# Optimization experiments

Hardware: AMD Instinct MI355X
Metric: run time of the kernel (lower is better)

The kernel has to match this reference:

```python
import jax, jax.numpy as jnp
import numpy as np
import math

N_HEAD = 16  # from init_kwargs

def setup_inputs() -> dict:
    key = jax.random.key(0)
    ks = jax.random.split(key, 11)
    B, T, D = 2, 2048, 1024
    s = 0.02
    return {
        "q": jax.random.normal(ks[0], (B, T, D), jnp.float32),
        "k": jax.random.normal(ks[1], (B, T, D), jnp.float32),
        "v": jax.random.normal(ks[2], (B, T, D), jnp.float32),
        "Wq": jax.random.normal(ks[3], (D, D), jnp.float32) * s,
        "bq": jax.random.normal(ks[4], (D,), jnp.float32) * s,
        "Wk": jax.random.normal(ks[5], (D, D), jnp.float32) * s,
        "bk": jax.random.normal(ks[6], (D,), jnp.float32) * s,
        "Wv": jax.random.normal(ks[7], (D, D), jnp.float32) * s,
        "bv": jax.random.normal(ks[8], (D,), jnp.float32) * s,
        "Wc": jax.random.normal(ks[9], (D, D), jnp.float32) * s,
        "bc": jax.random.normal(ks[10], (D,), jnp.float32) * s,
    }

def reference(q, k, v, Wq, bq, Wk, bk, Wv, bv, Wc, bc):
    B, T, D = q.shape
    H = N_HEAD
    nd = D // H

    def proj(x, W, b):
        # torch Linear: x @ W.T + b; then split heads -> [b, h, t, nd]
        y = x @ W.T + b
        return y.reshape(B, T, H, nd).transpose(0, 2, 1, 3)

    qh = proj(q, Wq, bq)
    kh = proj(k, Wk, bk)
    vh = proj(v, Wv, bv)

    # scores: [b, h, t_q, t_k]
    z = jnp.einsum('bhqd,bhkd->bhqk', qh, kh) / math.sqrt(nd)
    mask = jnp.tril(jnp.ones((T, T), dtype=bool))  # causal
    z = jnp.where(mask, z, -jnp.inf)
    # NOTE: original uses nn.Softmax(dim=-2) -> softmax over the QUERY axis
    attn = jax.nn.softmax(z, axis=-2)
    out = jnp.einsum('bhqk,bhkd->bhqd', attn, vh)  # [b, h, t, nd]
    out = out.transpose(0, 2, 1, 3).reshape(B, T, D)
    return out @ Wc.T + bc
```

## Files before the change

### kernel.cpp

```cpp
#include <hip/hip_runtime.h>


#define Dd 1024
#define Tt 2048
#define Bb 2
#define Hh 16
#define NDh 64
#define Mm (Bb * Tt)

using u16 = unsigned short;
using u32 = unsigned int;
typedef __attribute__((ext_vector_type(8))) short bf16x8;
typedef __attribute__((ext_vector_type(4))) float f32x4;

__device__ __forceinline__ u16 f2bf(float f) {
  return (u16)((__float_as_uint(f) + 0x8000u) >> 16);
}
__device__ __forceinline__ u32 pk2(float a, float b) {
  u32 ua = __float_as_uint(a) + 0x8000u;
  u32 ub = __float_as_uint(b) + 0x8000u;
  return __builtin_amdgcn_perm(ub, ua, 0x07060302u);
}
__device__ __forceinline__ void ldsdma16(const u16* g, u16* l) {
  __builtin_amdgcn_global_load_lds(
      (const __attribute__((address_space(1))) u32*)g,
      (__attribute__((address_space(3))) u32*)l, 16, 0, 0);
}
#define MFMA(a, b, c) __builtin_amdgcn_mfma_f32_16x16x32_bf16((a), (b), (c), 0, 0, 0)
__device__ __forceinline__ bf16x8 ldfrag(const u16* lds, int row, int kgrp) {
  return *(const bf16x8*)(lds + row * 64 + (((kgrp) ^ (row & 7)) * 8));
}

__global__ __launch_bounds__(256) void cvt_w(
    const float* __restrict__ w0, const float* __restrict__ w1,
    const float* __restrict__ w2, const float* __restrict__ w3,
    u16* __restrict__ dst, float* __restrict__ outz, float* __restrict__ lsumz)
{
  const int vid = blockIdx.x * 256 + threadIdx.x;
  const int seg = vid >> 18;
  const int off = (vid & 0x3FFFF) * 4;
  const float* s = seg == 0 ? w0 : seg == 1 ? w1 : seg == 2 ? w2 : w3;
  float4 f = *(const float4*)(s + off);
  ushort4 o;
  o.x = f2bf(f.x); o.y = f2bf(f.y); o.z = f2bf(f.z); o.w = f2bf(f.w);
  *(ushort4*)(dst + (size_t)seg * Dd * Dd + off) = o;
  *(float4*)(outz + (size_t)vid * 4) = make_float4(0.f, 0.f, 0.f, 0.f);
  if (vid < Bb * Hh * Tt / 4)
    *(float4*)(lsumz + (size_t)vid * 4) = make_float4(0.f, 0.f, 0.f, 0.f);
}

template <bool XF32>
__device__ __forceinline__ void gemm_body(
    const void* Xv, const u16* __restrict__ WB, const float* __restrict__ bias,
    void* Yv, float oscale, int omode, int kc, int knum, u16* As, u16* Bs)
{
  const int t = threadIdx.x, lane = t & 63, w = t >> 6;
  const int col = lane & 15, quad = lane >> 4;
  const int m0 = blockIdx.x * 64, n0 = blockIdx.y * 128;
  const int wm = (w >> 1) * 32, wn = (w & 1) * 64;
  const int drr = lane >> 3, dsw = ((lane & 7) ^ drr) * 8;
  const int ar = t >> 2, ag = (t & 3) * 2;
  const int kbeg = (Dd / knum) * kc, kend = kbeg + Dd / knum;

  f32x4 acc[2][4] = {};
  float4 xf[4];
  const float* X32 = (const float*)Xv;
  if constexpr (XF32) {
#pragma unroll
    for (int j = 0; j < 4; j++)
      xf[j] = ((const float4*)(X32 + (size_t)(m0 + ar) * Dd + kbeg + ag * 8))[j];
  }

  for (int k0 = kbeg; k0 < kend; k0 += 64) {
    __syncthreads();
#pragma unroll
    for (int i = 0; i < 4; i++) {
      const int rr = w * 32 + i * 8;
      ldsdma16(WB + (size_t)(n0 + rr + drr) * Dd + k0 + dsw, Bs + rr * 64);
    }
    if constexpr (XF32) {
      u32 pk[8];
#pragma unroll
      for (int j = 0; j < 4; j++) {
        pk[2 * j]     = pk2(xf[j].x, xf[j].y);
        pk[2 * j + 1] = pk2(xf[j].z, xf[j].w);
      }
      u16* dst = As + ar * 64;
      *(uint4*)(dst + ((ag ^ (ar & 7)) * 8))       = make_uint4(pk[0], pk[1], pk[2], pk[3]);
      *(uint4*)(dst + (((ag + 1) ^ (ar & 7)) * 8)) = make_uint4(pk[4], pk[5], pk[6], pk[7]);
      if (k0 + 64 < kend) {
#pragma unroll
        for (int j = 0; j < 4; j++)
          xf[j] = ((const float4*)(X32 + (size_t)(m0 + ar) * Dd + k0 + 64 + ag * 8))[j];
      }
    } else {
      const u16* X = (const u16*)Xv;
#pragma unroll
      for (int i = 0; i < 2; i++) {
        const int rr = w * 16 + i * 8;
        ldsdma16(X + (size_t)(m0 + rr + drr) * Dd + k0 + dsw, As + rr * 64);
      }
    }
    __syncthreads();
#pragma unroll
    for (int s = 0; s < 2; s++) {
      bf16x8 a[2], b[4];
#pragma unroll
      for (int i = 0; i < 2; i++)
        a[i] = ldfrag(As, wm + i * 16 + col, s * 4 + quad);
#pragma unroll
      for (int j = 0; j < 4; j++)
        b[j] = ldfrag(Bs, wn + j * 16 + col, s * 4 + quad);
#pragma unroll
      for (int i = 0; i < 2; i++)
#pragma unroll
        for (int j = 0; j < 4; j++)
          acc[i][j] = MFMA(a[i], b[j], acc[i][j]);
    }
  }

#pragma unroll
  for (int jt = 0; jt < 4; jt++) {
    const int n = n0 + wn + jt * 16 + col;
    const float bn = (omode == 2 && kc != 0) ? 0.f : bias[n];
    if (omode == 1) {
#pragma unroll
      for (int i = 0; i < 2; i++) {
        const int mg = m0 + wm + i * 16 + quad * 4;
        const int bb = mg >> 11, tl = mg & 2047;
        ushort4 o;
        o.x = f2bf(acc[i][jt][0] + bn);
        o.y = f2bf(acc[i][jt][1] + bn);
        o.z = f2bf(acc[i][jt][2] + bn);
        o.w = f2bf(acc[i][jt][3] + bn);
        *(ushort4*)((u16*)Yv + (size_t)bb * Dd * Tt + (size_t)n * Tt + tl) = o;
      }
    } else if (omode == 0) {
      u16* Y = (u16*)Yv;
#pragma unroll
      for (int i = 0; i < 2; i++)
#pragma unroll
        for (int r = 0; r < 4; r++) {
          const int m = m0 + wm + i * 16 + quad * 4 + r;
          Y[(size_t)m * Dd + n] = f2bf((acc[i][jt][r] + bn) * oscale);
        }
    } else {
      float* Y = (float*)Yv;
#pragma unroll
      for (int i = 0; i < 2; i++)
#pragma unroll
        for (int r = 0; r < 4; r++) {
          const int m = m0 + wm + i * 16 + quad * 4 + r;
          atomicAdd(&Y[(size_t)m * Dd + n], acc[i][jt][r] + bn);
        }
    }
  }
}

__global__ __launch_bounds__(256) void proj_qkv(
    const float* __restrict__ q, const float* __restrict__ k,
    const float* __restrict__ v, const u16* __restrict__ Wb,
    const float* __restrict__ bq, const float* __restrict__ bk,
    const float* __restrict__ bv,
    u16* __restrict__ Qp, u16* __restrict__ Kp, u16* __restrict__ VtG)
{
  __shared__ u16 As[64 * 64];
  __shared__ u16 Bs[128 * 64];
  const int z = blockIdx.z;
  const float* X = z == 0 ? q : z == 1 ? k : v;
  const u16* W = Wb + (size_t)z * Dd * Dd;
  const float* bias = z == 0 ? bq : z == 1 ? bk : bv;
  void* Y = z == 0 ? (void*)Qp : z == 1 ? (void*)Kp : (void*)VtG;
  gemm_body<true>(X, W, bias, Y, z == 0 ? 0.125f : 1.0f, z == 2 ? 1 : 0, 0, 1, As, Bs);
}

__global__ __launch_bounds__(256) void gemm_final(
    const u16* __restrict__ Ctx, const u16* __restrict__ Wcb,
    const float* __restrict__ bc, float* __restrict__ out)
{
  __shared__ u16 As[64 * 64];
  __shared__ u16 Bs[128 * 64];
  gemm_body<false>(Ctx, Wcb, bc, out, 1.0f, 2, blockIdx.z, 2, As, Bs);
}

__global__ __launch_bounds__(256) void attn_stats(
    const u16* __restrict__ Qp, const u16* __restrict__ Kp,
    float* __restrict__ lsum)
{
  __shared__ u16 Ks[128 * 64];
  __shared__ u16 Qs[64 * 64];
  const int t = threadIdx.x, lane = t & 63, w = t >> 6;
  const int col = lane & 15, quad = lane >> 4;
  const int bh = blockIdx.x, b = bh >> 4, h = bh & 15;
  const int j = blockIdx.y, tk0 = j * 128, c = blockIdx.z;
  const u16* Kbase = Kp + (size_t)b * Tt * Dd + h * NDh;
  const u16* Qbase = Qp + (size_t)b * Tt * Dd + h * NDh;
  const int drr = lane >> 3, dsw = ((lane & 7) ^ drr) * 8;

#pragma unroll
  for (int i = 0; i < 4; i++) {
    const int rr = w * 32 + i * 8;
    ldsdma16(Kbase + (size_t)(tk0 + rr + drr) * Dd + dsw, Ks + rr * 64);
  }
  __syncthreads();
  bf16x8 ka[2][2];
#pragma unroll
  for (int s2 = 0; s2 < 2; s2++) {
    const int row = w * 32 + s2 * 16 + col;
    ka[s2][0] = ldfrag(Ks, row, quad);
    ka[s2][1] = ldfrag(Ks, row, 4 + quad);
  }

  float l[2][4] = {};

  for (int d = 2 * j + c, i0 = 0; d < Tt / 64; d += 4, i0++) {
    const bool masked = (c < 2) && (i0 == 0);
    const int tq0 = d * 64;
    __syncthreads();
#pragma unroll
    for (int i = 0; i < 2; i++) {
      const int rr = w * 16 + i * 8;
      ldsdma16(Qbase + (size_t)(tq0 + rr + drr) * Dd + dsw, Qs + rr * 64);
    }
    __syncthreads();
#pragma unroll
    for (int jt = 0; jt < 4; jt++) {
      bf16x8 qb0 = ldfrag(Qs, jt * 16 + col, quad);
      bf16x8 qb1 = ldfrag(Qs, jt * 16 + col, 4 + quad);
      const int tq = tq0 + jt * 16 + col;
#pragma unroll
      for (int s2 = 0; s2 < 2; s2++) {
        f32x4 z = {};
        z = MFMA(ka[s2][0], qb0, z);
        z = MFMA(ka[s2][1], qb1, z);
#pragma unroll
        for (int r = 0; r < 4; r++) {
          float e = __expf(z[r]);
          if (masked) {
            const int tk = tk0 + w * 32 + s2 * 16 + quad * 4 + r;
            e = (tq >= tk) ? e : 0.f;
          }
          l[s2][r] += e;
        }
      }
    }
  }

#pragma unroll
  for (int s2 = 0; s2 < 2; s2++)
#pragma unroll
    for (int r = 0; r < 4; r++) {
      float s = l[s2][r];
#pragma unroll
      for (int m = 1; m < 16; m <<= 1) s += __shfl_xor(s, m);
      if (col == 0)
        atomicAdd(&lsum[(size_t)bh * Tt + tk0 + w * 32 + s2 * 16 + quad * 4 + r], s);
    }
}

__global__ __launch_bounds__(256) void attn_out(
    const u16* __restrict__ Qp, const u16* __restrict__ Kp,
    const u16* __restrict__ VtG, const float* __restrict__ lsum,
    u16* __restrict__ Ctx)
{
  __shared__ u16 QPs[64 * 64];
  __shared__ u16 Ks[64 * 64];
  __shared__ u16 Vts[64 * 64];
  __shared__ float srl[64];
  const int t = threadIdx.x, lane = t & 63, w = t >> 6;
  const int col = lane & 15, quad = lane >> 4;
  const int bh = blockIdx.x, b = bh >> 4, h = bh & 15;
  const int tq0 = (gridDim.y - 1 - blockIdx.y) * 64;
  const u16* Qbase = Qp + (size_t)b * Tt * Dd + h * NDh;
  const u16* Kbase = Kp + (size_t)b * Tt * Dd + h * NDh;
  const u16* Vbase = VtG + (size_t)b * Dd * Tt + (size_t)h * NDh * Tt;
  const int drr = lane >> 3, dsw = ((lane & 7) ^ drr) * 8;

#pragma unroll
  for (int i = 0; i < 2; i++) {
    const int rr = w * 16 + i * 8;
    ldsdma16(Qbase + (size_t)(tq0 + rr + drr) * Dd + dsw, QPs + rr * 64);
  }
  __syncthreads();
  bf16x8 qa[2];
  qa[0] = ldfrag(QPs, w * 16 + col, quad);
  qa[1] = ldfrag(QPs, w * 16 + col, 4 + quad);

  f32x4 o[4] = {};

  for (int tk0 = 0; tk0 <= tq0; tk0 += 64) {
    const bool masked = (tk0 == tq0);
    __syncthreads();
#pragma unroll
    for (int i = 0; i < 2; i++) {
      const int rr = w * 16 + i * 8;
      ldsdma16(Kbase + (size_t)(tk0 + rr + drr) * Dd + dsw, Ks + rr * 64);
      ldsdma16(Vbase + (size_t)(rr + drr) * Tt + tk0 + dsw, Vts + rr * 64);
    }
    if (t < 64) srl[t] = 1.0f / lsum[(size_t)bh * Tt + tk0 + t];
    __syncthreads();
#pragma unroll
    for (int jt = 0; jt < 4; jt++) {
      bf16x8 kb0 = ldfrag(Ks, jt * 16 + col, quad);
      bf16x8 kb1 = ldfrag(Ks, jt * 16 + col, 4 + quad);
      const int tkl = jt * 16 + col;
      const float rl = srl[tkl];
      f32x4 z = {};
      z = MFMA(qa[0], kb0, z);
      z = MFMA(qa[1], kb1, z);
#pragma unroll
      for (int r = 0; r < 4; r++) {
        const int row = w * 16 + quad * 4 + r;
        float p = __expf(z[r]) * rl;
        if (masked) p = (tkl <= row) ? p : 0.f;
        QPs[row * 64 + (((tkl >> 3) ^ (row & 7)) * 8) + (tkl & 7)] = f2bf(p);
      }
    }
    bf16x8 pa0 = ldfrag(QPs, w * 16 + col, quad);
    bf16x8 pa1 = ldfrag(QPs, w * 16 + col, 4 + quad);
#pragma unroll
    for (int dn = 0; dn < 4; dn++) {
      bf16x8 vb0 = ldfrag(Vts, dn * 16 + col, quad);
      bf16x8 vb1 = ldfrag(Vts, dn * 16 + col, 4 + quad);
      o[dn] = MFMA(pa0, vb0, o[dn]);
      o[dn] = MFMA(pa1, vb1, o[dn]);
    }
  }

#pragma unroll
  for (int dn = 0; dn < 4; dn++)
#pragma unroll
    for (int r = 0; r < 4; r++) {
      const int tq = tq0 + w * 16 + quad * 4 + r;
      Ctx[(size_t)(b * Tt + tq) * Dd + h * NDh + dn * 16 + col] = f2bf(o[dn][r]);
    }
}

extern "C" void kernel_launch(void* const* d_in, const int* in_sizes, int n_in,
                              void* d_out, int out_size, void* d_ws, size_t ws_size,
                              hipStream_t stream)
{
  const float* q  = (const float*)d_in[0];
  const float* k  = (const float*)d_in[1];
  const float* v  = (const float*)d_in[2];
  const float* Wq = (const float*)d_in[3];
  const float* bq = (const float*)d_in[4];
  const float* Wk = (const float*)d_in[5];
  const float* bk = (const float*)d_in[6];
  const float* Wv = (const float*)d_in[7];
  const float* bv = (const float*)d_in[8];
  const float* Wc = (const float*)d_in[9];
  const float* bc = (const float*)d_in[10];

  u16* Wb   = (u16*)d_ws;
  u16* Qp   = Wb + (size_t)4 * Dd * Dd;
  u16* Kp   = Qp + (size_t)Mm * Dd;
  u16* VtG  = Kp + (size_t)Mm * Dd;
  u16* Ctx  = VtG + (size_t)Mm * Dd;
  float* lsum = (float*)(Ctx + (size_t)Mm * Dd);

  cvt_w<<<4096, 256, 0, stream>>>(Wq, Wk, Wv, Wc, Wb, (float*)d_out, lsum);
  proj_qkv<<<dim3(Mm / 64, Dd / 128, 3), 256, 0, stream>>>(
      q, k, v, Wb, bq, bk, bv, Qp, Kp, VtG);
  attn_stats<<<dim3(Bb * Hh, Tt / 128, 4), 256, 0, stream>>>(Qp, Kp, lsum);
  attn_out<<<dim3(Bb * Hh, Tt / 64), 256, 0, stream>>>(Qp, Kp, VtG, lsum, Ctx);
  gemm_final<<<dim3(Mm / 64, Dd / 128, 2), 256, 0, stream>>>(
      Ctx, Wb + (size_t)3 * Dd * Dd, bc, (float*)d_out);
}
```

Baseline: 268.8 us.

## Pre-convert activations to bf16, enlarge GEMM and attention tiles, use exp2

The activation inputs are now converted to bf16 in the single conversion kernel, so the projection GEMM can stage both operands into shared memory with direct global-to-LDS loads. The GEMM tiles grow from 64x128 to 128x128, and the attention-stats and attention-output kernels process 128 query rows per block for more reuse of each K/V tile. The exp is replaced by a hardware exp2, with log2(e) folded into the Q scale. In exchange the code writes and rereads an extra bf16 copy of q/k/v, uses more registers and LDS per block, and launches fewer blocks, which may lower occupancy.

```diff
diff --git a/kernel.cpp b/kernel.cpp
--- a/kernel.cpp
+++ b/kernel.cpp
@@ -16,10 +16,8 @@
 __device__ __forceinline__ u16 f2bf(float f) {
   return (u16)((__float_as_uint(f) + 0x8000u) >> 16);
 }
-__device__ __forceinline__ u32 pk2(float a, float b) {
-  u32 ua = __float_as_uint(a) + 0x8000u;
-  u32 ub = __float_as_uint(b) + 0x8000u;
-  return __builtin_amdgcn_perm(ub, ua, 0x07060302u);
+__device__ __forceinline__ float fexp2(float x) {
+  return __builtin_amdgcn_exp2f(x);
 }
 __device__ __forceinline__ void ldsdma16(const u16* g, u16* l) {
   __builtin_amdgcn_global_load_lds(
@@ -31,88 +29,70 @@
   return *(const bf16x8*)(lds + row * 64 + (((kgrp) ^ (row & 7)) * 8));
 }
 
-__global__ __launch_bounds__(256) void cvt_w(
+__global__ __launch_bounds__(256) void cvt_all(
     const float* __restrict__ w0, const float* __restrict__ w1,
     const float* __restrict__ w2, const float* __restrict__ w3,
-    u16* __restrict__ dst, float* __restrict__ outz, float* __restrict__ lsumz)
+    const float* __restrict__ q, const float* __restrict__ k,
+    const float* __restrict__ v,
+    u16* __restrict__ Wb, u16* __restrict__ Xb,
+    float* __restrict__ outz, float* __restrict__ lsumz)
 {
   const int vid = blockIdx.x * 256 + threadIdx.x;
-  const int seg = vid >> 18;
-  const int off = (vid & 0x3FFFF) * 4;
-  const float* s = seg == 0 ? w0 : seg == 1 ? w1 : seg == 2 ? w2 : w3;
-  float4 f = *(const float4*)(s + off);
+  const float* s;
+  u16* d;
+  if (vid < (1 << 20)) {
+    const int seg = vid >> 18, off = (vid & 0x3FFFF) * 4;
+    s = (seg == 0 ? w0 : seg == 1 ? w1 : seg == 2 ? w2 : w3) + off;
+    d = Wb + (size_t)seg * Dd * Dd + off;
+    *(float4*)(outz + (size_t)vid * 4) = make_float4(0.f, 0.f, 0.f, 0.f);
+    if (vid < Bb * Hh * Tt / 4)
+      *(float4*)(lsumz + (size_t)vid * 4) = make_float4(0.f, 0.f, 0.f, 0.f);
+  } else {
+    const int iv = vid - (1 << 20);
+    const int seg = iv >> 20, off = (iv & 0xFFFFF) * 4;
+    s = (seg == 0 ? q : seg == 1 ? k : v) + off;
+    d = Xb + (size_t)seg * Mm * Dd + off;
+  }
+  float4 f = *(const float4*)s;
   ushort4 o;
   o.x = f2bf(f.x); o.y = f2bf(f.y); o.z = f2bf(f.z); o.w = f2bf(f.w);
-  *(ushort4*)(dst + (size_t)seg * Dd * Dd + off) = o;
-  *(float4*)(outz + (size_t)vid * 4) = make_float4(0.f, 0.f, 0.f, 0.f);
-  if (vid < Bb * Hh * Tt / 4)
-    *(float4*)(lsumz + (size_t)vid * 4) = make_float4(0.f, 0.f, 0.f, 0.f);
-}
-
-template <bool XF32>
+  *(ushort4*)d = o;
+}
+
 __device__ __forceinline__ void gemm_body(
-    const void* Xv, const u16* __restrict__ WB, const float* __restrict__ bias,
-    void* Yv, float oscale, int omode, int kc, int knum, u16* As, u16* Bs)
+    const u16* __restrict__ X, const u16* __restrict__ WB,
+    const float* __restrict__ bias, void* Yv, float oscale,
+    int omode, int kc, int knum, u16* As, u16* Bs)
 {
   const int t = threadIdx.x, lane = t & 63, w = t >> 6;
   const int col = lane & 15, quad = lane >> 4;
-  const int m0 = blockIdx.x * 64, n0 = blockIdx.y * 128;
-  const int wm = (w >> 1) * 32, wn = (w & 1) * 64;
+  const int m0 = blockIdx.x * 128, n0 = blockIdx.y * 128;
+  const int wm = (w >> 1) * 64, wn = (w & 1) * 64;
   const int drr = lane >> 3, dsw = ((lane & 7) ^ drr) * 8;
-  const int ar = t >> 2, ag = (t & 3) * 2;
   const int kbeg = (Dd / knum) * kc, kend = kbeg + Dd / knum;
 
-  f32x4 acc[2][4] = {};
-  float4 xf[4];
-  const float* X32 = (const float*)Xv;
-  if constexpr (XF32) {
-#pragma unroll
-    for (int j = 0; j < 4; j++)
-      xf[j] = ((const float4*)(X32 + (size_t)(m0 + ar) * Dd + kbeg + ag * 8))[j];
-  }
+  f32x4 acc[4][4] = {};
 
   for (int k0 = kbeg; k0 < kend; k0 += 64) {
     __syncthreads();
 #pragma unroll
     for (int i = 0; i < 4; i++) {
       const int rr = w * 32 + i * 8;
+      ldsdma16(X + (size_t)(m0 + rr + drr) * Dd + k0 + dsw, As + rr * 64);
       ldsdma16(WB + (size_t)(n0 + rr + drr) * Dd + k0 + dsw, Bs + rr * 64);
     }
-    if constexpr (XF32) {
-      u32 pk[8];
-#pragma unroll
-      for (int j = 0; j < 4; j++) {
-        pk[2 * j]     = pk2(xf[j].x, xf[j].y);
-        pk[2 * j + 1] = pk2(xf[j].z, xf[j].w);
-      }
-      u16* dst = As + ar * 64;
-      *(uint4*)(dst + ((ag ^ (ar & 7)) * 8))       = make_uint4(pk[0], pk[1], pk[2], pk[3]);
-      *(uint4*)(dst + (((ag + 1) ^ (ar & 7)) * 8)) = make_uint4(pk[4], pk[5], pk[6], pk[7]);
-      if (k0 + 64 < kend) {
-#pragma unroll
-        for (int j = 0; j < 4; j++)
-          xf[j] = ((const float4*)(X32 + (size_t)(m0 + ar) * Dd + k0 + 64 + ag * 8))[j];
-      }
-    } else {
-      const u16* X = (const u16*)Xv;
-#pragma unroll
-      for (int i = 0; i < 2; i++) {
-        const int rr = w * 16 + i * 8;
-        ldsdma16(X + (size_t)(m0 + rr + drr) * Dd + k0 + dsw, As + rr * 64);
-      }
-    }
     __syncthreads();
 #pragma unroll
     for (int s = 0; s < 2; s++) {
-      bf16x8 a[2], b[4];
-#pragma unroll
-      for (int i = 0; i < 2; i++)
+      bf16x8 a[4], b[4];
+#pragma unroll
+      for (int i = 0; i < 4; i++)
         a[i] = ldfrag(As, wm + i * 16 + col, s * 4 + quad);
 #pragma unroll
       for (int j = 0; j < 4; j++)
         b[j] = ldfrag(Bs, wn + j * 16 + col, s * 4 + quad);
 #pragma unroll
-      for (int i = 0; i < 2; i++)
+      for (int i = 0; i < 4; i++)
 #pragma unroll
         for (int j = 0; j < 4; j++)
           acc[i][j] = MFMA(a[i], b[j], acc[i][j]);
@@ -125,7 +105,7 @@
     const float bn = (omode == 2 && kc != 0) ? 0.f : bias[n];
     if (omode == 1) {
 #pragma unroll
-      for (int i = 0; i < 2; i++) {
+      for (int i = 0; i < 4; i++) {
         const int mg = m0 + wm + i * 16 + quad * 4;
         const int bb = mg >> 11, tl = mg & 2047;
         ushort4 o;
@@ -138,7 +118,7 @@
     } else if (omode == 0) {
       u16* Y = (u16*)Yv;
 #pragma unroll
-      for (int i = 0; i < 2; i++)
+      for (int i = 0; i < 4; i++)
 #pragma unroll
         for (int r = 0; r < 4; r++) {
           const int m = m0 + wm + i * 16 + quad * 4 + r;
@@ -147,7 +127,7 @@
     } else {
       float* Y = (float*)Yv;
 #pragma unroll
-      for (int i = 0; i < 2; i++)
+      for (int i = 0; i < 4; i++)
 #pragma unroll
         for (int r = 0; r < 4; r++) {
           const int m = m0 + wm + i * 16 + quad * 4 + r;
@@ -158,29 +138,29 @@
 }
 
 __global__ __launch_bounds__(256) void proj_qkv(
-    const float* __restrict__ q, const float* __restrict__ k,
-    const float* __restrict__ v, const u16* __restrict__ Wb,
+    const u16* __restrict__ Xb, const u16* __restrict__ Wb,
     const float* __restrict__ bq, const float* __restrict__ bk,
     const float* __restrict__ bv,
     u16* __restrict__ Qp, u16* __restrict__ Kp, u16* __restrict__ VtG)
 {
-  __shared__ u16 As[64 * 64];
+  __shared__ u16 As[128 * 64];
   __shared__ u16 Bs[128 * 64];
   const int z = blockIdx.z;
-  const float* X = z == 0 ? q : z == 1 ? k : v;
+  const u16* X = Xb + (size_t)z * Mm * Dd;
   const u16* W = Wb + (size_t)z * Dd * Dd;
   const float* bias = z == 0 ? bq : z == 1 ? bk : bv;
   void* Y = z == 0 ? (void*)Qp : z == 1 ? (void*)Kp : (void*)VtG;
-  gemm_body<true>(X, W, bias, Y, z == 0 ? 0.125f : 1.0f, z == 2 ? 1 : 0, 0, 1, As, Bs);
+  const float qs = 0.125f * 1.44269504088896f;
+  gemm_body(X, W, bias, Y, z == 0 ? qs : 1.0f, z == 2 ? 1 : 0, 0, 1, As, Bs);
 }
 
 __global__ __launch_bounds__(256) void gemm_final(
     const u16* __restrict__ Ctx, const u16* __restrict__ Wcb,
     const float* __restrict__ bc, float* __restrict__ out)
 {
-  __shared__ u16 As[64 * 64];
+  __shared__ u16 As[128 * 64];
   __shared__ u16 Bs[128 * 64];
-  gemm_body<false>(Ctx, Wcb, bc, out, 1.0f, 2, blockIdx.z, 2, As, Bs);
+  gemm_body(Ctx, Wcb, bc, out, 1.0f, 2, blockIdx.z, 2, As, Bs);
 }
 
 __global__ __launch_bounds__(256) void attn_stats(
@@ -188,7 +168,7 @@
     float* __restrict__ lsum)
 {
   __shared__ u16 Ks[128 * 64];
-  __shared__ u16 Qs[64 * 64];
+  __shared__ u16 Qs[128 * 64];
   const int t = threadIdx.x, lane = t & 63, w = t >> 6;
   const int col = lane & 15, quad = lane >> 4;
   const int bh = blockIdx.x, b = bh >> 4, h = bh & 15;
@@ -213,18 +193,18 @@
 
   float l[2][4] = {};
 
-  for (int d = 2 * j + c, i0 = 0; d < Tt / 64; d += 4, i0++) {
-    const bool masked = (c < 2) && (i0 == 0);
-    const int tq0 = d * 64;
-    __syncthreads();
-#pragma unroll
-    for (int i = 0; i < 2; i++) {
-      const int rr = w * 16 + i * 8;
+  for (int jj = j + c; jj < Tt / 128; jj += 2) {
+    const bool masked = (jj == j);
+    const int tq0 = jj * 128;
+    __syncthreads();
+#pragma unroll
+    for (int i = 0; i < 4; i++) {
+      const int rr = w * 32 + i * 8;
       ldsdma16(Qbase + (size_t)(tq0 + rr + drr) * Dd + dsw, Qs + rr * 64);
     }
     __syncthreads();
 #pragma unroll
-    for (int jt = 0; jt < 4; jt++) {
+    for (int jt = 0; jt < 8; jt++) {
       bf16x8 qb0 = ldfrag(Qs, jt * 16 + col, quad);
       bf16x8 qb1 = ldfrag(Qs, jt * 16 + col, 4 + quad);
       const int tq = tq0 + jt * 16 + col;
@@ -235,7 +215,7 @@
         z = MFMA(ka[s2][1], qb1, z);
 #pragma unroll
         for (int r = 0; r < 4; r++) {
-          float e = __expf(z[r]);
+          float e = fexp2(z[r]);
           if (masked) {
             const int tk = tk0 + w * 32 + s2 * 16 + quad * 4 + r;
             e = (tq >= tk) ? e : 0.f;
@@ -263,33 +243,37 @@
     const u16* __restrict__ VtG, const float* __restrict__ lsum,
     u16* __restrict__ Ctx)
 {
-  __shared__ u16 QPs[64 * 64];
+  __shared__ u16 QPs[128 * 64];
   __shared__ u16 Ks[64 * 64];
   __shared__ u16 Vts[64 * 64];
   __shared__ float srl[64];
   const int t = threadIdx.x, lane = t & 63, w = t >> 6;
   const int col = lane & 15, quad = lane >> 4;
   const int bh = blockIdx.x, b = bh >> 4, h = bh & 15;
-  const int tq0 = (gridDim.y - 1 - blockIdx.y) * 64;
+  const int tq0 = (gridDim.y - 1 - blockIdx.y) * 128;
   const u16* Qbase = Qp + (size_t)b * Tt * Dd + h * NDh;
   const u16* Kbase = Kp + (size_t)b * Tt * Dd + h * NDh;
   const u16* Vbase = VtG + (size_t)b * Dd * Tt + (size_t)h * NDh * Tt;
   const int drr = lane >> 3, dsw = ((lane & 7) ^ drr) * 8;
 
 #pragma unroll
-  for (int i = 0; i < 2; i++) {
-    const int rr = w * 16 + i * 8;
+  for (int i = 0; i < 4; i++) {
+    const int rr = w * 32 + i * 8;
     ldsdma16(Qbase + (size_t)(tq0 + rr + drr) * Dd + dsw, QPs + rr * 64);
   }
   __syncthreads();
-  bf16x8 qa[2];
-  qa[0] = ldfrag(QPs, w * 16 + col, quad);
-  qa[1] = ldfrag(QPs, w * 16 + col, 4 + quad);
-
-  f32x4 o[4] = {};
-
-  for (int tk0 = 0; tk0 <= tq0; tk0 += 64) {
-    const bool masked = (tk0 == tq0);
+  bf16x8 qa[2][2];
+#pragma unroll
+  for (int s2 = 0; s2 < 2; s2++) {
+    const int row = w * 32 + s2 * 16 + col;
+    qa[s2][0] = ldfrag(QPs, row, quad);
+    qa[s2][1] = ldfrag(QPs, row, 4 + quad);
+  }
+
+  f32x4 o[2][4] = {};
+
+  for (int tk0 = 0; tk0 < tq0 + 128; tk0 += 64) {
+    const bool masked = (tk0 >= tq0);
     __syncthreads();
 #pragma unroll
     for (int i = 0; i < 2; i++) {
@@ -305,35 +289,48 @@
       bf16x8 kb1 = ldfrag(Ks, jt * 16 + col, 4 + quad);
       const int tkl = jt * 16 + col;
       const float rl = srl[tkl];
-      f32x4 z = {};
-      z = MFMA(qa[0], kb0, z);
-      z = MFMA(qa[1], kb1, z);
-#pragma unroll
-      for (int r = 0; r < 4; r++) {
-        const int row = w * 16 + quad * 4 + r;
-        float p = __expf(z[r]) * rl;
-        if (masked) p = (tkl <= row) ? p : 0.f;
-        QPs[row * 64 + (((tkl >> 3) ^ (row & 7)) * 8) + (tkl & 7)] = f2bf(p);
-      }
-    }
-    bf16x8 pa0 = ldfrag(QPs, w * 16 + col, quad);
-    bf16x8 pa1 = ldfrag(QPs, w * 16 + col, 4 + quad);
+#pragma unroll
+      for (int s2 = 0; s2 < 2; s2++) {
+        f32x4 z = {};
+        z = MFMA(qa[s2][0], kb0, z);
+        z = MFMA(qa[s2][1], kb1, z);
+#pragma unroll
+        for (int r = 0; r < 4; r++) {
+          const int row = w * 32 + s2 * 16 + quad * 4 + r;
+          float p = fexp2(z[r]) * rl;
+          if (masked) p = (tk0 + tkl <= tq0 + row) ? p : 0.f;
+          QPs[row * 64 + (((tkl >> 3) ^ (row & 7)) * 8) + (tkl & 7)] = f2bf(p);
+        }
+      }
+    }
+    bf16x8 pa[2][2];
+#pragma unroll
+    for (int s2 = 0; s2 < 2; s2++) {
+      const int row = w * 32 + s2 * 16 + col;
+      pa[s2][0] = ldfrag(QPs, row, quad);
+      pa[s2][1] = ldfrag(QPs, row, 4 + quad);
+    }
 #pragma unroll
     for (int dn = 0; dn < 4; dn++) {
       bf16x8 vb0 = ldfrag(Vts, dn * 16 + col, quad);
       bf16x8 vb1 = ldfrag(Vts, dn * 16 + col, 4 + quad);
-      o[dn] = MFMA(pa0, vb0, o[dn]);
-      o[dn] = MFMA(pa1, vb1, o[dn]);
-    }
-  }
-
-#pragma unroll
-  for (int dn = 0; dn < 4; dn++)
-#pragma unroll
-    for (int r = 0; r < 4; r++) {
-      const int tq = tq0 + w * 16 + quad * 4 + r;
-      Ctx[(size_t)(b * Tt + tq) * Dd + h * NDh + dn * 16 + col] = f2bf(o[dn][r]);
-    }
+#pragma unroll
+      for (int s2 = 0; s2 < 2; s2++) {
+        o[s2][dn] = MFMA(pa[s2][0], vb0, o[s2][dn]);
+        o[s2][dn] = MFMA(pa[s2][1], vb1, o[s2][dn]);
+      }
+    }
+  }
+
+#pragma unroll
+  for (int s2 = 0; s2 < 2; s2++)
+#pragma unroll
+    for (int dn = 0; dn < 4; dn++)
+#pragma unroll
+      for (int r = 0; r < 4; r++) {
+        const int tq = tq0 + w * 32 + s2 * 16 + quad * 4 + r;
+        Ctx[(size_t)(b * Tt + tq) * Dd + h * NDh + dn * 16 + col] = f2bf(o[s2][dn][r]);
+      }
 }
 
 extern "C" void kernel_launch(void* const* d_in, const int* in_sizes, int n_in,
@@ -353,17 +350,19 @@
   const float* bc = (const float*)d_in[10];
 
   u16* Wb   = (u16*)d_ws;
-  u16* Qp   = Wb + (size_t)4 * Dd * Dd;
+  u16* Xb   = Wb + (size_t)4 * Dd * Dd;
+  u16* Qp   = Xb + (size_t)3 * Mm * Dd;
   u16* Kp   = Qp + (size_t)Mm * Dd;
   u16* VtG  = Kp + (size_t)Mm * Dd;
   u16* Ctx  = VtG + (size_t)Mm * Dd;
   float* lsum = (float*)(Ctx + (size_t)Mm * Dd);
 
-  cvt_w<<<4096, 256, 0, stream>>>(Wq, Wk, Wv, Wc, Wb, (float*)d_out, lsum);
-  proj_qkv<<<dim3(Mm / 64, Dd / 128, 3), 256, 0, stream>>>(
-      q, k, v, Wb, bq, bk, bv, Qp, Kp, VtG);
-  attn_stats<<<dim3(Bb * Hh, Tt / 128, 4), 256, 0, stream>>>(Qp, Kp, lsum);
-  attn_out<<<dim3(Bb * Hh, Tt / 64), 256, 0, stream>>>(Qp, Kp, VtG, lsum, Ctx);
-  gemm_final<<<dim3(Mm / 64, Dd / 128, 2), 256, 0, stream>>>(
+  cvt_all<<<16384, 256, 0, stream>>>(Wq, Wk, Wv, Wc, q, k, v, Wb, Xb,
+                                     (float*)d_out, lsum);
+  proj_qkv<<<dim3(Mm / 128, Dd / 128, 3), 256, 0, stream>>>(
+      Xb, Wb, bq, bk, bv, Qp, Kp, VtG);
+  attn_stats<<<dim3(Bb * Hh, Tt / 128, 2), 256, 0, stream>>>(Qp, Kp, lsum);
+  attn_out<<<dim3(Bb * Hh, Tt / 128), 256, 0, stream>>>(Qp, Kp, VtG, lsum, Ctx);
+  gemm_final<<<dim3(Mm / 128, Dd / 128, 2), 256, 0, stream>>>(
       Ctx, Wb + (size_t)3 * Dd * Dd, bc, (float*)d_out);
 }
```

Result: slower. 276.3 us (+2.8%).
